# Kernel optimization log

Measured on AMD Instinct MI355X. Metric: run time of the kernel, lower is better.

The kernel has to match this reference:

```python
import jax, jax.numpy as jnp
import numpy as np

B, R, N, D_IN, D_OUT = 8, 4, 1024, 256, 256


def setup_inputs() -> dict:
    key = jax.random.key(0)
    k1, k2, k3, k4 = jax.random.split(key, 4)
    text = jax.random.normal(k1, (B, N, D_IN), dtype=jnp.float32)
    adj = jax.random.uniform(k2, (B, R, N, N), dtype=jnp.float32)
    weight = jax.random.normal(k3, (R, D_IN, D_OUT), dtype=jnp.float32) * 0.02
    bias = jax.random.normal(k4, (D_OUT,), dtype=jnp.float32) * 0.02
    return {"text": text, "adj": adj, "weight": weight, "bias": bias}


def reference(text, adj, weight, bias):
    # Row-normalize adjacency per relation (diag_embed+matmul in torch == row scale).
    rowsum = adj.sum(axis=-1)                                   # [B,R,N]
    r_inv = jnp.where(rowsum == 0, 0.0, 1.0 / rowsum)           # inf -> 0
    norm_adj = adj * r_inv[..., None]                           # [B,R,N,N]
    # Per-relation message passing, batched over relations.
    hidden = jnp.einsum('brij,bjd->brid', norm_adj, text)       # [B,R,N,D_in]
    # Concat over relations along feature dim: [B,N,R*D_in]
    tmp = jnp.transpose(hidden, (0, 2, 1, 3)).reshape(text.shape[0], text.shape[1], -1)
    w = weight.reshape(-1, weight.shape[-1])                    # [R*D_in, D_out]
    return tmp @ w + bias
```

## Files before the change

### kernel.cpp

```cpp
#include <hip/hip_runtime.h>
#include <hip/hip_bf16.h>
#include <stdint.h>

typedef __bf16 bf16_8 __attribute__((ext_vector_type(8)));
typedef float f32x4 __attribute__((ext_vector_type(4)));
typedef unsigned int u32;
typedef unsigned short u16;


__device__ __forceinline__ u16 f2b(float f) {
    return __builtin_bit_cast(u16, __float2bfloat16(f));
}

__device__ __forceinline__ u32 swz_off(u32 row, u32 g) {
    return (row * 4u + (g ^ ((row >> 1) & 3u))) * 16u;
}

__device__ __forceinline__ void gload_lds16(const void* g, void* l) {
    __builtin_amdgcn_global_load_lds((const __attribute__((address_space(1))) void*)g,
                                     (__attribute__((address_space(3))) void*)l, 16, 0, 0);
}

__device__ __forceinline__ void memfence_sched() { asm volatile("" ::: "memory"); }

__device__ __forceinline__ uint4 pack8(float4 a, float4 b) {
    uint4 pk;
    pk.x = (u32)f2b(a.x) | ((u32)f2b(a.y) << 16);
    pk.y = (u32)f2b(a.z) | ((u32)f2b(a.w) << 16);
    pk.z = (u32)f2b(b.x) | ((u32)f2b(b.y) << 16);
    pk.w = (u32)f2b(b.z) | ((u32)f2b(b.w) << 16);
    return pk;
}

template <int KSTEPS>
__device__ __forceinline__ void gemm_core(const u16* pA, u32 strideA,
                                          const u16* pB, u32 strideB,
                                          char* smem, f32x4 acc[4][4]) {
    const u32 t    = threadIdx.x;
    const u32 lane = t & 63u;
    const u32 w    = t >> 6;
    const u32 wm   = (w >> 1) * 64u;
    const u32 wn   = (w & 1u) * 64u;
    const u32 waveByte = (t & 192u) * 16u;
    const u32 row0 = t >> 2;
    const u32 gg0  = (t & 3u) ^ ((row0 >> 1) & 3u);
    const u32 row1 = row0 + 64u;
    const u32 gg1  = ((t + 256u) & 3u) ^ ((row1 >> 1) & 3u);
    const u32 fr = lane & 15u;
    const u32 fg = lane >> 4;

    gload_lds16(pA + (size_t)row0 * strideA + gg0 * 8u, smem + waveByte);
    gload_lds16(pA + (size_t)row1 * strideA + gg1 * 8u, smem + waveByte + 4096u);
    gload_lds16(pB + (size_t)row0 * strideB + gg0 * 8u, smem + 16384u + waveByte);
    gload_lds16(pB + (size_t)row1 * strideB + gg1 * 8u, smem + 16384u + waveByte + 4096u);
    asm volatile("s_waitcnt vmcnt(0)" ::: "memory");
    __builtin_amdgcn_s_barrier();

    u32 c = 0;
#pragma unroll 2
    for (int ks = 0; ks < KSTEPS; ++ks) {
        char* curA = smem + c * 8192u;
        char* curB = smem + 16384u + c * 8192u;
        if (ks + 1 < KSTEPS) {
            char* nxtA = smem + (c ^ 1u) * 8192u;
            char* nxtB = smem + 16384u + (c ^ 1u) * 8192u;
            const u32 k0 = (u32)(ks + 1) * 32u;
            gload_lds16(pA + (size_t)row0 * strideA + k0 + gg0 * 8u, nxtA + waveByte);
            gload_lds16(pA + (size_t)row1 * strideA + k0 + gg1 * 8u, nxtA + waveByte + 4096u);
            gload_lds16(pB + (size_t)row0 * strideB + k0 + gg0 * 8u, nxtB + waveByte);
            gload_lds16(pB + (size_t)row1 * strideB + k0 + gg1 * 8u, nxtB + waveByte + 4096u);
        }

        bf16_8 af[4], bfv[4];
#pragma unroll
        for (int mt = 0; mt < 4; ++mt) {
            uint4 v = *(const uint4*)(curA + swz_off(wm + (u32)mt * 16u + fr, fg));
            af[mt] = __builtin_bit_cast(bf16_8, v);
        }
#pragma unroll
        for (int nt = 0; nt < 4; ++nt) {
            uint4 v = *(const uint4*)(curB + swz_off(wn + (u32)nt * 16u + fr, fg));
            bfv[nt] = __builtin_bit_cast(bf16_8, v);
        }
#pragma unroll
        for (int mt = 0; mt < 4; ++mt)
#pragma unroll
            for (int nt = 0; nt < 4; ++nt)
                acc[mt][nt] = __builtin_amdgcn_mfma_f32_16x16x32_bf16(af[mt], bfv[nt],
                                                                      acc[mt][nt], 0, 0, 0);

        if (ks + 1 < KSTEPS) {
            asm volatile("s_waitcnt vmcnt(0)" ::: "memory");
            __builtin_amdgcn_s_barrier();
        }
        c ^= 1u;
    }
}

__global__ __launch_bounds__(256) void text_cvt_kernel(const float* t, u16* tb) {
    const u32 i8 = blockIdx.x * 256u + threadIdx.x;
    const float4 a = ((const float4*)t)[i8 * 2u];
    const float4 b = ((const float4*)t)[i8 * 2u + 1u];
    ((uint4*)tb)[i8] = pack8(a, b);
}

__global__ __launch_bounds__(256) void wt_cvt_kernel(const float* W, u16* Wt) {
    const u32 idx = blockIdx.x * 256u + threadIdx.x;
    const u32 r = idx >> 16, rem = idx & 65535u, dout = rem >> 8, din = rem & 255u;
    Wt[idx] = f2b(W[(r << 16) + (din << 8) + dout]);
}

__global__ __launch_bounds__(256) void y_gemm_kernel(const u16* Wt, const u16* textb,
                                                     u16* Yt) {
    __shared__ char smem[32768];
    const u32 bx = blockIdx.x;
    const u32 n0 = (bx & 7u) * 128u;
    const u32 m0 = ((bx >> 3) & 1u) * 128u;
    const u32 r  = (bx >> 4) & 3u;
    const u32 b  = bx >> 6;
    const u16* pA = Wt + (size_t)r * 65536u + (size_t)m0 * 256u;
    const u16* pB = textb + (size_t)b * 262144u + (size_t)n0 * 256u;
    f32x4 acc[4][4];
#pragma unroll
    for (int i = 0; i < 4; ++i)
#pragma unroll
        for (int j = 0; j < 4; ++j) acc[i][j] = (f32x4){0.f, 0.f, 0.f, 0.f};
    gemm_core<8>(pA, 256u, pB, 256u, smem, acc);

    const u32 lane = threadIdx.x & 63u, w = threadIdx.x >> 6;
    const u32 wm = (w >> 1) * 64u, wn = (w & 1u) * 64u;
    const u32 rit = (lane >> 4) * 4u, cit = lane & 15u;
    u16* yb = Yt + (size_t)(b * 4u + r) * 262144u;
#pragma unroll
    for (int mt = 0; mt < 4; ++mt)
#pragma unroll
        for (int nt = 0; nt < 4; ++nt) {
            const u32 m = m0 + wm + (u32)mt * 16u + rit;
            const u32 n = n0 + wn + (u32)nt * 16u + cit;
#pragma unroll
            for (int rg = 0; rg < 4; ++rg)
                yb[(size_t)(m + (u32)rg) * 1024u + n] = f2b(acc[mt][nt][rg]);
        }
}

__global__ __launch_bounds__(512, 4) void adj_gemm_partial(const float* adj,
                                                           const u16* Yt,
                                                           float* partial) {
    __shared__ char smem[57600];
    char* bufA = smem;
    char* bufB = smem + 8192;
    float* sInv = (float*)(smem + 57344);

    const u32 raw = blockIdx.x;
    const u32 bx = (raw & 7u) * 64u + (raw >> 3);

    const u32 i0 = (bx & 15u) * 64u;
    const u32 r  = (bx >> 4) & 3u;
    const u32 b  = bx >> 6;

    const float* pA = adj + (size_t)(b * 4u + r) * 1048576u + (size_t)i0 * 1024u;
    const u16*   pB = Yt + (size_t)(b * 4u + r) * 262144u;

    const u32 t    = threadIdx.x;
    const u32 lane = t & 63u;
    const u32 w    = t >> 6;
    const u32 wi   = (w >> 1) * 16u;
    const u32 wd   = (w & 1u) * 128u;
    const u32 fr   = lane & 15u;
    const u32 fg   = lane >> 4;

    const u32 arow = t >> 3;
    const u32 acg  = ((t >> 1) & 3u) ^ ((arow >> 1) & 3u);
    const float* aPtr = pA + (size_t)arow * 1024u + acg * 8u + (t & 1u) * 4u;

    const u32 brow0 = t >> 2;
    const u32 brow1 = (t + 512u) >> 2;
    const u32 bcg0  = (t & 3u) ^ ((brow0 >> 1) & 3u);
    const u32 bcg1  = (t & 3u) ^ ((brow1 >> 1) & 3u);
    const u16* bPtr0 = pB + (size_t)brow0 * 1024u + bcg0 * 8u;
    const u16* bPtr1 = pB + (size_t)brow1 * 1024u + bcg1 * 8u;
    const u32 waveB = (t & 448u) * 16u;

    f32x4 acc[8];
#pragma unroll
    for (int i = 0; i < 8; ++i) acc[i] = (f32x4){0.f, 0.f, 0.f, 0.f};

    float s0 = 0.f;
    float4 rA[2];

    auto stageB = [&](u32 kt, char* dst) {
        gload_lds16(bPtr0 + kt * 32u, dst + waveB);
        gload_lds16(bPtr1 + kt * 32u, dst + 8192u + waveB);
    };
    auto packA = [&](float4 a, char* dst) {
        s0 += (a.x + a.y) + (a.z + a.w);
        uint2 pk;
        pk.x = (u32)f2b(a.x) | ((u32)f2b(a.y) << 16);
        pk.y = (u32)f2b(a.z) | ((u32)f2b(a.w) << 16);
        *(uint2*)(dst + t * 8u) = pk;
    };
    auto do_mfma = [&](char* curA, char* curB) {
        uint4 va = *(const uint4*)(curA + swz_off(wi + fr, fg));
        bf16_8 af = __builtin_bit_cast(bf16_8, va);
#pragma unroll
        for (int nt = 0; nt < 8; ++nt) {
            uint4 v = *(const uint4*)(curB + swz_off(wd + (u32)nt * 16u + fr, fg));
            bf16_8 bfv = __builtin_bit_cast(bf16_8, v);
            acc[nt] = __builtin_amdgcn_mfma_f32_16x16x32_bf16(af, bfv, acc[nt], 0, 0, 0);
        }
    };

    rA[0] = *(const float4*)(aPtr);
    stageB(0u, bufB);
    memfence_sched();
    rA[1] = *(const float4*)(aPtr + 32u);
    stageB(1u, bufB + 16384u);
    memfence_sched();
    packA(rA[0], bufA);
    asm volatile("s_waitcnt vmcnt(3) lgkmcnt(0)" ::: "memory");
    __builtin_amdgcn_s_barrier();

#pragma unroll 6
    for (int ks = 0; ks < 30; ++ks) {
        const int cA = ks & 1;
        const int nA = cA ^ 1;

        packA(rA[nA], bufA + (u32)nA * 4096u);
        rA[cA] = *(const float4*)(aPtr + (u32)(ks + 2) * 32u);
        stageB((u32)(ks + 2), bufB + (u32)((ks + 2) % 3) * 16384u);

        do_mfma(bufA + (u32)cA * 4096u, bufB + (u32)(ks % 3) * 16384u);

        asm volatile("s_waitcnt vmcnt(3) lgkmcnt(0)" ::: "memory");
        __builtin_amdgcn_s_barrier();
    }

    packA(rA[1], bufA + 4096u);
    do_mfma(bufA, bufB);
    asm volatile("s_waitcnt vmcnt(0) lgkmcnt(0)" ::: "memory");
    __builtin_amdgcn_s_barrier();

    do_mfma(bufA + 4096u, bufB + 16384u);

    s0 += __shfl_down(s0, 4, 64);
    s0 += __shfl_down(s0, 2, 64);
    s0 += __shfl_down(s0, 1, 64);
    if ((t & 7u) == 0u) sInv[arow] = (s0 == 0.f) ? 0.f : 1.f / s0;
    __syncthreads();

    const u32 rit = fg * 4u;
    float* pp = partial + (size_t)(b * 4u + r) * 262144u + (size_t)i0 * 256u;
#pragma unroll
    for (int rg = 0; rg < 4; ++rg) {
        const u32 mRow = wi + rit + (u32)rg;
        const float inv = sInv[mRow];
#pragma unroll
        for (int nt = 0; nt < 8; ++nt)
            pp[(size_t)mRow * 256u + wd + (u32)nt * 16u + fr] = acc[nt][rg] * inv;
    }
}

__global__ __launch_bounds__(256) void reduce_kernel(const float* partial,
                                                     const float* bias, float* out) {
    const u32 i4 = blockIdx.x * 256u + threadIdx.x;
    const u32 base = i4 * 4u;
    const u32 b = base >> 18;
    const u32 rem = base & 262143u;
    float4 s = ((const float4*)bias)[i4 & 63u];
#pragma unroll
    for (u32 r = 0; r < 4; ++r) {
        const float4 v = *(const float4*)(partial + (((size_t)(b * 4u + r)) << 18) + rem);
        s.x += v.x; s.y += v.y; s.z += v.z; s.w += v.w;
    }
    ((float4*)out)[i4] = s;
}

extern "C" void kernel_launch(void* const* d_in, const int* in_sizes, int n_in,
                              void* d_out, int out_size, void* d_ws, size_t ws_size,
                              hipStream_t stream) {
    const float* text = (const float*)d_in[0];
    const float* adj  = (const float*)d_in[1];
    const float* wgt  = (const float*)d_in[2];
    const float* bias = (const float*)d_in[3];
    float* out = (float*)d_out;

    char* ws = (char*)d_ws;
    u16* Yt        = (u16*)ws;
    u16* textb     = (u16*)(ws + 16777216u);
    u16* Wt        = (u16*)(ws + 20971520u);
    float* partial = (float*)(ws + 21495808u);

    text_cvt_kernel<<<1024, 256, 0, stream>>>(text, textb);
    wt_cvt_kernel<<<1024, 256, 0, stream>>>(wgt, Wt);
    y_gemm_kernel<<<512, 256, 0, stream>>>(Wt, textb, Yt);
    adj_gemm_partial<<<512, 512, 0, stream>>>(adj, Yt, partial);
    reduce_kernel<<<2048, 256, 0, stream>>>(partial, bias, out);
}
```

Measured before the change: 67.09 us.

## Enlarge adj GEMM tile to 128x256 with K=64 phased pipeline

Rewrites the adjacency GEMM to use 128-row by 256-column tiles with a 64-wide K step, 8 waves in a 2x4 layout each computing 64x64. The main loop is split into four phases per K tile, with interleaved staging loads, barriers and s_setprio around the MFMA blocks. The goal is more reuse of the B operand per block and fewer K iterations. In exchange it uses 128KB of LDS and a lower occupancy target, and launches only 256 blocks, which may underfill the GPU's compute units.

```diff
diff --git a/kernel.cpp b/kernel.cpp
--- a/kernel.cpp
+++ b/kernel.cpp
@@ -14,6 +14,10 @@
 
 __device__ __forceinline__ u32 swz_off(u32 row, u32 g) {
     return (row * 4u + (g ^ ((row >> 1) & 3u))) * 16u;
+}
+
+__device__ __forceinline__ u32 swz8(u32 row, u32 c) {
+    return (row * 8u + (c ^ ((row >> 1) & 7u))) * 16u;
 }
 
 __device__ __forceinline__ void gload_lds16(const void* g, void* l) {
@@ -143,121 +147,166 @@
         }
 }
 
-__global__ __launch_bounds__(512, 4) void adj_gemm_partial(const float* adj,
-                                                           const u16* Yt,
-                                                           float* partial) {
-    __shared__ char smem[57600];
+__global__ __launch_bounds__(512, 2) void adj_gemm_8ph(const float* adj, const u16* Yt,
+                                                       float* partial) {
+    __shared__ char smem[131072];
     char* bufA = smem;
-    char* bufB = smem + 8192;
-    float* sInv = (float*)(smem + 57344);
+    char* bufB = smem + 32768;
+    float* sInv = (float*)smem;
 
     const u32 raw = blockIdx.x;
-    const u32 bx = (raw & 7u) * 64u + (raw >> 3);
-
-    const u32 i0 = (bx & 15u) * 64u;
-    const u32 r  = (bx >> 4) & 3u;
-    const u32 b  = bx >> 6;
+    const u32 bx = (raw & 7u) * 32u + (raw >> 3);
+    const u32 it = bx & 7u;
+    const u32 r  = (bx >> 3) & 3u;
+    const u32 b  = bx >> 5;
+    const u32 i0 = it * 128u;
 
     const float* pA = adj + (size_t)(b * 4u + r) * 1048576u + (size_t)i0 * 1024u;
     const u16*   pB = Yt + (size_t)(b * 4u + r) * 262144u;
 
-    const u32 t    = threadIdx.x;
-    const u32 lane = t & 63u;
-    const u32 w    = t >> 6;
-    const u32 wi   = (w >> 1) * 16u;
-    const u32 wd   = (w & 1u) * 128u;
-    const u32 fr   = lane & 15u;
-    const u32 fg   = lane >> 4;
-
-    const u32 arow = t >> 3;
-    const u32 acg  = ((t >> 1) & 3u) ^ ((arow >> 1) & 3u);
-    const float* aPtr = pA + (size_t)arow * 1024u + acg * 8u + (t & 1u) * 4u;
-
-    const u32 brow0 = t >> 2;
-    const u32 brow1 = (t + 512u) >> 2;
-    const u32 bcg0  = (t & 3u) ^ ((brow0 >> 1) & 3u);
-    const u32 bcg1  = (t & 3u) ^ ((brow1 >> 1) & 3u);
-    const u16* bPtr0 = pB + (size_t)brow0 * 1024u + bcg0 * 8u;
-    const u16* bPtr1 = pB + (size_t)brow1 * 1024u + bcg1 * 8u;
+    const u32 t = threadIdx.x, lane = t & 63u, w = t >> 6;
+    const u32 wm = (w >> 2) * 64u;
+    const u32 wn = (w & 3u) * 64u;
+    const u32 fr = lane & 15u, fg = lane >> 4;
+
+    const u32 sRow = t >> 2;
+    const float* aBase = pA + (size_t)sRow * 1024u + (t & 3u) * 16u;
+    const u32 aSw = (sRow >> 1) & 7u;
+    const u32 aSlot0 = (sRow * 8u + (((t & 3u) * 2u) ^ aSw)) * 16u;
+    const u32 aSlot1 = (sRow * 8u + (((t & 3u) * 2u + 1u) ^ aSw)) * 16u;
+
+    u32 bOff[4];
+#pragma unroll
+    for (int j = 0; j < 4; ++j) {
+        const u32 ci = (u32)j * 512u + t;
+        const u32 row = ci >> 3, g = ci & 7u;
+        bOff[j] = row * 1024u + (g ^ ((row >> 1) & 7u)) * 8u;
+    }
     const u32 waveB = (t & 448u) * 16u;
 
-    f32x4 acc[8];
-#pragma unroll
-    for (int i = 0; i < 8; ++i) acc[i] = (f32x4){0.f, 0.f, 0.f, 0.f};
+    f32x4 acc[4][4];
+#pragma unroll
+    for (int i = 0; i < 4; ++i)
+#pragma unroll
+        for (int j = 0; j < 4; ++j) acc[i][j] = (f32x4){0.f, 0.f, 0.f, 0.f};
 
     float s0 = 0.f;
-    float4 rA[2];
-
-    auto stageB = [&](u32 kt, char* dst) {
-        gload_lds16(bPtr0 + kt * 32u, dst + waveB);
-        gload_lds16(bPtr1 + kt * 32u, dst + 8192u + waveB);
+    float4 rA[2][4];
+
+    auto loadA = [&](float4* dst, u32 kt) {
+        const float* p = aBase + kt * 64u;
+        dst[0] = *(const float4*)(p);
+        dst[1] = *(const float4*)(p + 4);
+        dst[2] = *(const float4*)(p + 8);
+        dst[3] = *(const float4*)(p + 12);
     };
-    auto packA = [&](float4 a, char* dst) {
-        s0 += (a.x + a.y) + (a.z + a.w);
-        uint2 pk;
-        pk.x = (u32)f2b(a.x) | ((u32)f2b(a.y) << 16);
-        pk.y = (u32)f2b(a.z) | ((u32)f2b(a.w) << 16);
-        *(uint2*)(dst + t * 8u) = pk;
+    auto packA = [&](const float4* rs, char* dst) {
+        s0 += (rs[0].x + rs[0].y + rs[0].z + rs[0].w)
+            + (rs[1].x + rs[1].y + rs[1].z + rs[1].w)
+            + (rs[2].x + rs[2].y + rs[2].z + rs[2].w)
+            + (rs[3].x + rs[3].y + rs[3].z + rs[3].w);
+        *(uint4*)(dst + aSlot0) = pack8(rs[0], rs[1]);
+        *(uint4*)(dst + aSlot1) = pack8(rs[2], rs[3]);
     };
-    auto do_mfma = [&](char* curA, char* curB) {
-        uint4 va = *(const uint4*)(curA + swz_off(wi + fr, fg));
-        bf16_8 af = __builtin_bit_cast(bf16_8, va);
-#pragma unroll
-        for (int nt = 0; nt < 8; ++nt) {
-            uint4 v = *(const uint4*)(curB + swz_off(wd + (u32)nt * 16u + fr, fg));
-            bf16_8 bfv = __builtin_bit_cast(bf16_8, v);
-            acc[nt] = __builtin_amdgcn_mfma_f32_16x16x32_bf16(af, bfv, acc[nt], 0, 0, 0);
+
+    auto ktile = [&](char* bufAc, char* bufBc, char* bufAn, char* bufBn,
+                     float4* rIssue, const float4* rPack, u32 ktIss,
+                     bool doIssue, bool doPack, bool lastTile) {
+        bf16_8 af[4][2];
+#pragma unroll
+        for (int p = 0; p < 4; ++p) {
+            if (p == 0) {
+                if (doIssue) { loadA(rIssue, ktIss); memfence_sched(); }
+#pragma unroll
+                for (int mt = 0; mt < 4; ++mt)
+#pragma unroll
+                    for (int ks = 0; ks < 2; ++ks) {
+                        uint4 v = *(const uint4*)(bufAc +
+                                   swz8(wm + (u32)mt * 16u + fr, (u32)ks * 4u + fg));
+                        af[mt][ks] = __builtin_bit_cast(bf16_8, v);
+                    }
+            }
+            if (doIssue) {
+                gload_lds16(pB + bOff[p] + ktIss * 64u,
+                            bufBn + (u32)p * 8192u + waveB);
+                memfence_sched();
+            }
+            if (p == 3 && doPack) packA(rPack, bufAn);
+
+            bf16_8 bf[2];
+#pragma unroll
+            for (int ks = 0; ks < 2; ++ks) {
+                uint4 v = *(const uint4*)(bufBc +
+                           swz8(wn + (u32)p * 16u + fr, (u32)ks * 4u + fg));
+                bf[ks] = __builtin_bit_cast(bf16_8, v);
+            }
+            __builtin_amdgcn_s_barrier();
+            __builtin_amdgcn_s_setprio(1);
+#pragma unroll
+            for (int mt = 0; mt < 4; ++mt)
+#pragma unroll
+                for (int ks = 0; ks < 2; ++ks)
+                    acc[mt][p] = __builtin_amdgcn_mfma_f32_16x16x32_bf16(
+                        af[mt][ks], bf[ks], acc[mt][p], 0, 0, 0);
+            __builtin_amdgcn_s_setprio(0);
+            if (p < 3) {
+                __builtin_amdgcn_s_barrier();
+            } else {
+                if (doIssue)
+                    asm volatile("s_waitcnt vmcnt(8) lgkmcnt(0)" ::: "memory");
+                else if (doPack)
+                    asm volatile("s_waitcnt vmcnt(0) lgkmcnt(0)" ::: "memory");
+                else
+                    asm volatile("s_waitcnt lgkmcnt(0)" ::: "memory");
+                if (!lastTile) __builtin_amdgcn_s_barrier();
+            }
         }
     };
 
-    rA[0] = *(const float4*)(aPtr);
-    stageB(0u, bufB);
+    loadA(rA[0], 0u);
     memfence_sched();
-    rA[1] = *(const float4*)(aPtr + 32u);
-    stageB(1u, bufB + 16384u);
+#pragma unroll
+    for (int j = 0; j < 4; ++j)
+        gload_lds16(pB + bOff[j], bufB + (u32)j * 8192u + waveB);
+    memfence_sched();
+    loadA(rA[1], 1u);
+    memfence_sched();
+#pragma unroll
+    for (int j = 0; j < 4; ++j)
+        gload_lds16(pB + bOff[j] + 64u, bufB + 32768u + (u32)j * 8192u + waveB);
     memfence_sched();
     packA(rA[0], bufA);
-    asm volatile("s_waitcnt vmcnt(3) lgkmcnt(0)" ::: "memory");
+    asm volatile("s_waitcnt vmcnt(8) lgkmcnt(0)" ::: "memory");
     __builtin_amdgcn_s_barrier();
 
-#pragma unroll 6
-    for (int ks = 0; ks < 30; ++ks) {
-        const int cA = ks & 1;
-        const int nA = cA ^ 1;
-
-        packA(rA[nA], bufA + (u32)nA * 4096u);
-        rA[cA] = *(const float4*)(aPtr + (u32)(ks + 2) * 32u);
-        stageB((u32)(ks + 2), bufB + (u32)((ks + 2) % 3) * 16384u);
-
-        do_mfma(bufA + (u32)cA * 4096u, bufB + (u32)(ks % 3) * 16384u);
-
-        asm volatile("s_waitcnt vmcnt(3) lgkmcnt(0)" ::: "memory");
-        __builtin_amdgcn_s_barrier();
+#pragma unroll 2
+    for (int kt = 0; kt < 14; ++kt) {
+        const u32 cA = (u32)kt & 1u, nA = cA ^ 1u;
+        ktile(bufA + cA * 16384u, bufB + (u32)(kt % 3) * 32768u,
+              bufA + nA * 16384u, bufB + (u32)((kt + 2) % 3) * 32768u,
+              rA[cA], rA[nA], (u32)(kt + 2), true, true, false);
     }
-
-    packA(rA[1], bufA + 4096u);
-    do_mfma(bufA, bufB);
-    asm volatile("s_waitcnt vmcnt(0) lgkmcnt(0)" ::: "memory");
-    __builtin_amdgcn_s_barrier();
-
-    do_mfma(bufA + 4096u, bufB + 16384u);
-
-    s0 += __shfl_down(s0, 4, 64);
+    ktile(bufA, bufB + 2u * 32768u, bufA + 16384u, bufB,
+          rA[0], rA[1], 0u, false, true, false);
+    ktile(bufA + 16384u, bufB, bufA, bufB,
+          rA[0], rA[1], 0u, false, false, true);
+
     s0 += __shfl_down(s0, 2, 64);
     s0 += __shfl_down(s0, 1, 64);
-    if ((t & 7u) == 0u) sInv[arow] = (s0 == 0.f) ? 0.f : 1.f / s0;
+    if ((t & 3u) == 0u) sInv[sRow] = (s0 == 0.f) ? 0.f : 1.f / s0;
     __syncthreads();
 
-    const u32 rit = fg * 4u;
     float* pp = partial + (size_t)(b * 4u + r) * 262144u + (size_t)i0 * 256u;
 #pragma unroll
-    for (int rg = 0; rg < 4; ++rg) {
-        const u32 mRow = wi + rit + (u32)rg;
-        const float inv = sInv[mRow];
-#pragma unroll
-        for (int nt = 0; nt < 8; ++nt)
-            pp[(size_t)mRow * 256u + wd + (u32)nt * 16u + fr] = acc[nt][rg] * inv;
-    }
+    for (int mt = 0; mt < 4; ++mt)
+#pragma unroll
+        for (int rg = 0; rg < 4; ++rg) {
+            const u32 mRow = wm + (u32)mt * 16u + fg * 4u + (u32)rg;
+            const float inv = sInv[mRow];
+#pragma unroll
+            for (int nt = 0; nt < 4; ++nt)
+                pp[(size_t)mRow * 256u + wn + (u32)nt * 16u + fr] = acc[mt][nt][rg] * inv;
+        }
 }
 
 __global__ __launch_bounds__(256) void reduce_kernel(const float* partial,
@@ -293,6 +342,6 @@
     text_cvt_kernel<<<1024, 256, 0, stream>>>(text, textb);
     wt_cvt_kernel<<<1024, 256, 0, stream>>>(wgt, Wt);
     y_gemm_kernel<<<512, 256, 0, stream>>>(Wt, textb, Yt);
-    adj_gemm_partial<<<512, 512, 0, stream>>>(adj, Yt, partial);
+    adj_gemm_8ph<<<256, 512, 0, stream>>>(adj, Yt, partial);
     reduce_kernel<<<2048, 256, 0, stream>>>(partial, bias, out);
 }
```

New measurement: 82.04 us. 1.22x slower.

## Fuse relation reduction and bias into adj GEMM, drop reduce kernel

Applied to the files above, without the earlier changes.

Each block now processes a 32-row tile across all four relations sequentially, scaling each relation's result by its row-normalization and accumulating in registers before adding bias and writing the final output. This removes the fp32 partial buffer round trip and the separate reduce launch. In exchange the grid halves to 256 blocks with smaller tiles per block, reducing parallelism and per-iteration MFMA work relative to loads.

```diff
diff --git a/kernel.cpp b/kernel.cpp
--- a/kernel.cpp
+++ b/kernel.cpp
@@ -143,136 +143,120 @@
         }
 }
 
-__global__ __launch_bounds__(512, 4) void adj_gemm_partial(const float* adj,
-                                                           const u16* Yt,
-                                                           float* partial) {
-    __shared__ char smem[57600];
+__global__ __launch_bounds__(512, 2) void adj_gemm_out(const float* adj, const u16* Yt,
+                                                       const float* bias, float* out) {
+    __shared__ char smem[53376];
     char* bufA = smem;
-    char* bufB = smem + 8192;
-    float* sInv = (float*)(smem + 57344);
+    char* bufB = smem + 4096;
+    float* sInv = (float*)(smem + 53248);
 
     const u32 raw = blockIdx.x;
-    const u32 bx = (raw & 7u) * 64u + (raw >> 3);
-
-    const u32 i0 = (bx & 15u) * 64u;
-    const u32 r  = (bx >> 4) & 3u;
-    const u32 b  = bx >> 6;
-
-    const float* pA = adj + (size_t)(b * 4u + r) * 1048576u + (size_t)i0 * 1024u;
-    const u16*   pB = Yt + (size_t)(b * 4u + r) * 262144u;
-
-    const u32 t    = threadIdx.x;
-    const u32 lane = t & 63u;
-    const u32 w    = t >> 6;
-    const u32 wi   = (w >> 1) * 16u;
-    const u32 wd   = (w & 1u) * 128u;
-    const u32 fr   = lane & 15u;
-    const u32 fg   = lane >> 4;
-
-    const u32 arow = t >> 3;
-    const u32 acg  = ((t >> 1) & 3u) ^ ((arow >> 1) & 3u);
-    const float* aPtr = pA + (size_t)arow * 1024u + acg * 8u + (t & 1u) * 4u;
+    const u32 bx = (raw & 7u) * 32u + (raw >> 3);
+    const u32 i0 = (bx & 31u) * 32u;
+    const u32 b  = bx >> 5;
+
+    const u32 t = threadIdx.x, lane = t & 63u, w = t >> 6;
+    const u32 wi = (w >> 2) * 16u;
+    const u32 wd = (w & 3u) * 64u;
+    const u32 fr = lane & 15u, fg = lane >> 4;
+
+    const u32 sRow = t >> 4;
+    const u32 aKoff = (((t >> 2) & 3u) ^ ((sRow >> 1) & 3u)) * 8u + (t & 3u) * 2u;
 
     const u32 brow0 = t >> 2;
     const u32 brow1 = (t + 512u) >> 2;
-    const u32 bcg0  = (t & 3u) ^ ((brow0 >> 1) & 3u);
-    const u32 bcg1  = (t & 3u) ^ ((brow1 >> 1) & 3u);
-    const u16* bPtr0 = pB + (size_t)brow0 * 1024u + bcg0 * 8u;
-    const u16* bPtr1 = pB + (size_t)brow1 * 1024u + bcg1 * 8u;
+    const u32 bg0 = (t & 3u) ^ ((brow0 >> 1) & 3u);
+    const u32 bg1 = (t & 3u) ^ ((brow1 >> 1) & 3u);
     const u32 waveB = (t & 448u) * 16u;
 
-    f32x4 acc[8];
-#pragma unroll
-    for (int i = 0; i < 8; ++i) acc[i] = (f32x4){0.f, 0.f, 0.f, 0.f};
-
-    float s0 = 0.f;
-    float4 rA[2];
-
-    auto stageB = [&](u32 kt, char* dst) {
-        gload_lds16(bPtr0 + kt * 32u, dst + waveB);
-        gload_lds16(bPtr1 + kt * 32u, dst + 8192u + waveB);
-    };
-    auto packA = [&](float4 a, char* dst) {
-        s0 += (a.x + a.y) + (a.z + a.w);
-        uint2 pk;
-        pk.x = (u32)f2b(a.x) | ((u32)f2b(a.y) << 16);
-        pk.y = (u32)f2b(a.z) | ((u32)f2b(a.w) << 16);
-        *(uint2*)(dst + t * 8u) = pk;
-    };
-    auto do_mfma = [&](char* curA, char* curB) {
-        uint4 va = *(const uint4*)(curA + swz_off(wi + fr, fg));
-        bf16_8 af = __builtin_bit_cast(bf16_8, va);
-#pragma unroll
-        for (int nt = 0; nt < 8; ++nt) {
-            uint4 v = *(const uint4*)(curB + swz_off(wd + (u32)nt * 16u + fr, fg));
-            bf16_8 bfv = __builtin_bit_cast(bf16_8, v);
-            acc[nt] = __builtin_amdgcn_mfma_f32_16x16x32_bf16(af, bfv, acc[nt], 0, 0, 0);
-        }
-    };
-
-    rA[0] = *(const float4*)(aPtr);
-    stageB(0u, bufB);
-    memfence_sched();
-    rA[1] = *(const float4*)(aPtr + 32u);
-    stageB(1u, bufB + 16384u);
-    memfence_sched();
-    packA(rA[0], bufA);
-    asm volatile("s_waitcnt vmcnt(3) lgkmcnt(0)" ::: "memory");
-    __builtin_amdgcn_s_barrier();
-
-#pragma unroll 6
-    for (int ks = 0; ks < 30; ++ks) {
-        const int cA = ks & 1;
-        const int nA = cA ^ 1;
-
-        packA(rA[nA], bufA + (u32)nA * 4096u);
-        rA[cA] = *(const float4*)(aPtr + (u32)(ks + 2) * 32u);
-        stageB((u32)(ks + 2), bufB + (u32)((ks + 2) % 3) * 16384u);
-
-        do_mfma(bufA + (u32)cA * 4096u, bufB + (u32)(ks % 3) * 16384u);
-
+    f32x4 accT[4], accR[4];
+#pragma unroll
+    for (int i = 0; i < 4; ++i) accT[i] = (f32x4){0.f, 0.f, 0.f, 0.f};
+
+#pragma unroll 1
+    for (u32 r = 0; r < 4u; ++r) {
+        const float* pAr = adj + (((size_t)(b * 4u + r)) << 20) + (size_t)i0 * 1024u;
+        const u16*   pBr = Yt + (((size_t)(b * 4u + r)) << 18);
+        const float* aSrc = pAr + (size_t)sRow * 1024u + aKoff;
+        const u16* b0p = pBr + (size_t)brow0 * 1024u + bg0 * 8u;
+        const u16* b1p = pBr + (size_t)brow1 * 1024u + bg1 * 8u;
+
+#pragma unroll
+        for (int i = 0; i < 4; ++i) accR[i] = (f32x4){0.f, 0.f, 0.f, 0.f};
+        float s0 = 0.f;
+        float2 rA[2];
+
+        auto stageB = [&](u32 kt, char* dst) {
+            gload_lds16(b0p + kt * 32u, dst + waveB);
+            gload_lds16(b1p + kt * 32u, dst + 8192u + waveB);
+        };
+        auto packA = [&](float2 a, char* dst) {
+            s0 += a.x + a.y;
+            *(u32*)(dst + t * 4u) = (u32)f2b(a.x) | ((u32)f2b(a.y) << 16);
+        };
+        auto do_mfma = [&](char* curA, char* curB) {
+            uint4 va = *(const uint4*)(curA + swz_off(wi + fr, fg));
+            bf16_8 af = __builtin_bit_cast(bf16_8, va);
+#pragma unroll
+            for (int nt = 0; nt < 4; ++nt) {
+                uint4 v = *(const uint4*)(curB + swz_off(wd + (u32)nt * 16u + fr, fg));
+                bf16_8 bfv = __builtin_bit_cast(bf16_8, v);
+                accR[nt] = __builtin_amdgcn_mfma_f32_16x16x32_bf16(af, bfv, accR[nt],
+                                                                   0, 0, 0);
+            }
+        };
+
+        rA[0] = *(const float2*)(aSrc);
+        stageB(0u, bufB);
+        memfence_sched();
+        rA[1] = *(const float2*)(aSrc + 32u);
+        stageB(1u, bufB + 16384u);
+        memfence_sched();
+        packA(rA[0], bufA);
         asm volatile("s_waitcnt vmcnt(3) lgkmcnt(0)" ::: "memory");
         __builtin_amdgcn_s_barrier();
+
+#pragma unroll 6
+        for (int ks = 0; ks < 30; ++ks) {
+            const u32 cA = (u32)ks & 1u, nA = cA ^ 1u;
+            packA(rA[nA], bufA + nA * 2048u);
+            rA[cA] = *(const float2*)(aSrc + (u32)(ks + 2) * 32u);
+            stageB((u32)(ks + 2), bufB + (u32)((ks + 2) % 3) * 16384u);
+            do_mfma(bufA + cA * 2048u, bufB + (u32)(ks % 3) * 16384u);
+            asm volatile("s_waitcnt vmcnt(3) lgkmcnt(0)" ::: "memory");
+            __builtin_amdgcn_s_barrier();
+        }
+        packA(rA[1], bufA + 2048u);
+        do_mfma(bufA, bufB);
+        asm volatile("s_waitcnt vmcnt(0) lgkmcnt(0)" ::: "memory");
+        __builtin_amdgcn_s_barrier();
+        do_mfma(bufA + 2048u, bufB + 16384u);
+
+        s0 += __shfl_down(s0, 8, 16);
+        s0 += __shfl_down(s0, 4, 16);
+        s0 += __shfl_down(s0, 2, 16);
+        s0 += __shfl_down(s0, 1, 16);
+        if ((t & 15u) == 0u) sInv[sRow] = (s0 == 0.f) ? 0.f : 1.f / s0;
+        __syncthreads();
+#pragma unroll
+        for (int rg = 0; rg < 4; ++rg) {
+            const float inv = sInv[wi + fg * 4u + (u32)rg];
+#pragma unroll
+            for (int nt = 0; nt < 4; ++nt) accT[nt][rg] += accR[nt][rg] * inv;
+        }
     }
 
-    packA(rA[1], bufA + 4096u);
-    do_mfma(bufA, bufB);
-    asm volatile("s_waitcnt vmcnt(0) lgkmcnt(0)" ::: "memory");
-    __builtin_amdgcn_s_barrier();
-
-    do_mfma(bufA + 4096u, bufB + 16384u);
-
-    s0 += __shfl_down(s0, 4, 64);
-    s0 += __shfl_down(s0, 2, 64);
-    s0 += __shfl_down(s0, 1, 64);
-    if ((t & 7u) == 0u) sInv[arow] = (s0 == 0.f) ? 0.f : 1.f / s0;
-    __syncthreads();
-
-    const u32 rit = fg * 4u;
-    float* pp = partial + (size_t)(b * 4u + r) * 262144u + (size_t)i0 * 256u;
-#pragma unroll
-    for (int rg = 0; rg < 4; ++rg) {
-        const u32 mRow = wi + rit + (u32)rg;
-        const float inv = sInv[mRow];
-#pragma unroll
-        for (int nt = 0; nt < 8; ++nt)
-            pp[(size_t)mRow * 256u + wd + (u32)nt * 16u + fr] = acc[nt][rg] * inv;
+    float* ob = out + ((size_t)b << 18) + (size_t)i0 * 256u;
+#pragma unroll
+    for (int nt = 0; nt < 4; ++nt) {
+        const u32 col = wd + (u32)nt * 16u + fr;
+        const float bv = bias[col];
+#pragma unroll
+        for (int rg = 0; rg < 4; ++rg) {
+            const u32 mRow = wi + fg * 4u + (u32)rg;
+            ob[(size_t)mRow * 256u + col] = accT[nt][rg] + bv;
+        }
     }
-}
-
-__global__ __launch_bounds__(256) void reduce_kernel(const float* partial,
-                                                     const float* bias, float* out) {
-    const u32 i4 = blockIdx.x * 256u + threadIdx.x;
-    const u32 base = i4 * 4u;
-    const u32 b = base >> 18;
-    const u32 rem = base & 262143u;
-    float4 s = ((const float4*)bias)[i4 & 63u];
-#pragma unroll
-    for (u32 r = 0; r < 4; ++r) {
-        const float4 v = *(const float4*)(partial + (((size_t)(b * 4u + r)) << 18) + rem);
-        s.x += v.x; s.y += v.y; s.z += v.z; s.w += v.w;
-    }
-    ((float4*)out)[i4] = s;
 }
 
 extern "C" void kernel_launch(void* const* d_in, const int* in_sizes, int n_in,
@@ -285,14 +269,12 @@
     float* out = (float*)d_out;
 
     char* ws = (char*)d_ws;
-    u16* Yt        = (u16*)ws;
-    u16* textb     = (u16*)(ws + 16777216u);
-    u16* Wt        = (u16*)(ws + 20971520u);
-    float* partial = (float*)(ws + 21495808u);
+    u16* Yt    = (u16*)ws;
+    u16* textb = (u16*)(ws + 16777216u);
+    u16* Wt    = (u16*)(ws + 20971520u);
 
     text_cvt_kernel<<<1024, 256, 0, stream>>>(text, textb);
     wt_cvt_kernel<<<1024, 256, 0, stream>>>(wgt, Wt);
     y_gemm_kernel<<<512, 256, 0, stream>>>(Wt, textb, Yt);
-    adj_gemm_partial<<<512, 512, 0, stream>>>(adj, Yt, partial);
-    reduce_kernel<<<2048, 256, 0, stream>>>(partial, bias, out);
-}
+    adj_gemm_out<<<256, 512, 0, stream>>>(adj, Yt, bias, out);
+}
```

Result: slower. 108.8 us (+62.1%).

## Enlarge adj GEMM block tile to 128 rows with 4x4 per-wave MFMA tiles

Applied to the files above, without the earlier changes.

Each adj_gemm_partial block now covers 128 adjacency rows instead of 64, using a 2x4 wave layout where every wave computes a 64x64 tile with a 4x4 grid of MFMAs. The goal is to cut redundant reloads of the Yt operand, which halve because there are half as many blocks, and to raise the MFMA-to-LDS-read ratio per wave. The cost is larger LDS use, more accumulator registers, lower occupancy (launch bounds 2), and only 256 blocks, which may underfill the CUs. The pack8 helper is assumed to exist in the hidden part of the file.

```diff
diff --git a/kernel.cpp b/kernel.cpp
--- a/kernel.cpp
+++ b/kernel.cpp
@@ -143,121 +143,124 @@
         }
 }
 
-__global__ __launch_bounds__(512, 4) void adj_gemm_partial(const float* adj,
+__global__ __launch_bounds__(512, 2) void adj_gemm_partial(const float* adj,
                                                            const u16* Yt,
                                                            float* partial) {
-    __shared__ char smem[57600];
+    __shared__ char smem[66048];
     char* bufA = smem;
-    char* bufB = smem + 8192;
-    float* sInv = (float*)(smem + 57344);
+    char* bufB = smem + 16384;
+    float* sInv = (float*)(smem + 65536);
 
     const u32 raw = blockIdx.x;
-    const u32 bx = (raw & 7u) * 64u + (raw >> 3);
-
-    const u32 i0 = (bx & 15u) * 64u;
-    const u32 r  = (bx >> 4) & 3u;
-    const u32 b  = bx >> 6;
-
-    const float* pA = adj + (size_t)(b * 4u + r) * 1048576u + (size_t)i0 * 1024u;
-    const u16*   pB = Yt + (size_t)(b * 4u + r) * 262144u;
-
-    const u32 t    = threadIdx.x;
-    const u32 lane = t & 63u;
-    const u32 w    = t >> 6;
-    const u32 wi   = (w >> 1) * 16u;
-    const u32 wd   = (w & 1u) * 128u;
-    const u32 fr   = lane & 15u;
-    const u32 fg   = lane >> 4;
-
-    const u32 arow = t >> 3;
-    const u32 acg  = ((t >> 1) & 3u) ^ ((arow >> 1) & 3u);
-    const float* aPtr = pA + (size_t)arow * 1024u + acg * 8u + (t & 1u) * 4u;
+    const u32 bx = (raw & 7u) * 32u + (raw >> 3);
+    const u32 i0 = (bx & 7u) * 128u;
+    const u32 r  = (bx >> 3) & 3u;
+    const u32 b  = bx >> 5;
+
+    const float* pA = adj + (((size_t)(b * 4u + r)) << 20) + (size_t)i0 * 1024u;
+    const u16*   pB = Yt + (((size_t)(b * 4u + r)) << 18);
+
+    const u32 t = threadIdx.x, lane = t & 63u, w = t >> 6;
+    const u32 wm = (w >> 2) * 64u;
+    const u32 wn = (w & 3u) * 64u;
+    const u32 fr = lane & 15u, fg = lane >> 4;
+
+    const u32 sRow = t >> 2;
+    const u32 cSwz = (t & 3u) ^ ((sRow >> 1) & 3u);
+    const float* aSrc = pA + (size_t)sRow * 1024u + cSwz * 8u;
 
     const u32 brow0 = t >> 2;
     const u32 brow1 = (t + 512u) >> 2;
-    const u32 bcg0  = (t & 3u) ^ ((brow0 >> 1) & 3u);
-    const u32 bcg1  = (t & 3u) ^ ((brow1 >> 1) & 3u);
-    const u16* bPtr0 = pB + (size_t)brow0 * 1024u + bcg0 * 8u;
-    const u16* bPtr1 = pB + (size_t)brow1 * 1024u + bcg1 * 8u;
+    const u32 bg0 = (t & 3u) ^ ((brow0 >> 1) & 3u);
+    const u32 bg1 = (t & 3u) ^ ((brow1 >> 1) & 3u);
+    const u16* b0p = pB + (size_t)brow0 * 1024u + bg0 * 8u;
+    const u16* b1p = pB + (size_t)brow1 * 1024u + bg1 * 8u;
     const u32 waveB = (t & 448u) * 16u;
 
-    f32x4 acc[8];
-#pragma unroll
-    for (int i = 0; i < 8; ++i) acc[i] = (f32x4){0.f, 0.f, 0.f, 0.f};
+    f32x4 acc[4][4];
+#pragma unroll
+    for (int i = 0; i < 4; ++i)
+#pragma unroll
+        for (int j = 0; j < 4; ++j) acc[i][j] = (f32x4){0.f, 0.f, 0.f, 0.f};
 
     float s0 = 0.f;
-    float4 rA[2];
-
+    float4 rA[2][2];
+
+    auto loadA = [&](float4* dst, u32 kt) {
+        dst[0] = *(const float4*)(aSrc + kt * 32u);
+        dst[1] = *(const float4*)(aSrc + kt * 32u + 4u);
+    };
     auto stageB = [&](u32 kt, char* dst) {
-        gload_lds16(bPtr0 + kt * 32u, dst + waveB);
-        gload_lds16(bPtr1 + kt * 32u, dst + 8192u + waveB);
+        gload_lds16(b0p + kt * 32u, dst + waveB);
+        gload_lds16(b1p + kt * 32u, dst + 8192u + waveB);
     };
-    auto packA = [&](float4 a, char* dst) {
-        s0 += (a.x + a.y) + (a.z + a.w);
-        uint2 pk;
-        pk.x = (u32)f2b(a.x) | ((u32)f2b(a.y) << 16);
-        pk.y = (u32)f2b(a.z) | ((u32)f2b(a.w) << 16);
-        *(uint2*)(dst + t * 8u) = pk;
+    auto packA = [&](const float4* a2, char* dst) {
+        s0 += (a2[0].x + a2[0].y + a2[0].z + a2[0].w)
+            + (a2[1].x + a2[1].y + a2[1].z + a2[1].w);
+        *(uint4*)(dst + t * 16u) = pack8(a2[0], a2[1]);
     };
     auto do_mfma = [&](char* curA, char* curB) {
-        uint4 va = *(const uint4*)(curA + swz_off(wi + fr, fg));
-        bf16_8 af = __builtin_bit_cast(bf16_8, va);
-#pragma unroll
-        for (int nt = 0; nt < 8; ++nt) {
-            uint4 v = *(const uint4*)(curB + swz_off(wd + (u32)nt * 16u + fr, fg));
-            bf16_8 bfv = __builtin_bit_cast(bf16_8, v);
-            acc[nt] = __builtin_amdgcn_mfma_f32_16x16x32_bf16(af, bfv, acc[nt], 0, 0, 0);
-        }
+        bf16_8 af[4], bfv[4];
+#pragma unroll
+        for (int mt = 0; mt < 4; ++mt) {
+            uint4 v = *(const uint4*)(curA + swz_off(wm + (u32)mt * 16u + fr, fg));
+            af[mt] = __builtin_bit_cast(bf16_8, v);
+        }
+#pragma unroll
+        for (int nt = 0; nt < 4; ++nt) {
+            uint4 v = *(const uint4*)(curB + swz_off(wn + (u32)nt * 16u + fr, fg));
+            bfv[nt] = __builtin_bit_cast(bf16_8, v);
+        }
+#pragma unroll
+        for (int mt = 0; mt < 4; ++mt)
+#pragma unroll
+            for (int nt = 0; nt < 4; ++nt)
+                acc[mt][nt] = __builtin_amdgcn_mfma_f32_16x16x32_bf16(af[mt], bfv[nt],
+                                                                      acc[mt][nt], 0, 0, 0);
     };
 
-    rA[0] = *(const float4*)(aPtr);
+    loadA(rA[0], 0u);
     stageB(0u, bufB);
     memfence_sched();
-    rA[1] = *(const float4*)(aPtr + 32u);
+    loadA(rA[1], 1u);
     stageB(1u, bufB + 16384u);
     memfence_sched();
     packA(rA[0], bufA);
-    asm volatile("s_waitcnt vmcnt(3) lgkmcnt(0)" ::: "memory");
+    asm volatile("s_waitcnt vmcnt(4) lgkmcnt(0)" ::: "memory");
     __builtin_amdgcn_s_barrier();
 
 #pragma unroll 6
     for (int ks = 0; ks < 30; ++ks) {
-        const int cA = ks & 1;
-        const int nA = cA ^ 1;
-
-        packA(rA[nA], bufA + (u32)nA * 4096u);
-        rA[cA] = *(const float4*)(aPtr + (u32)(ks + 2) * 32u);
+        const u32 cA = (u32)ks & 1u, nA = cA ^ 1u;
+        packA(rA[nA], bufA + nA * 8192u);
+        loadA(rA[cA], (u32)(ks + 2));
         stageB((u32)(ks + 2), bufB + (u32)((ks + 2) % 3) * 16384u);
-
-        do_mfma(bufA + (u32)cA * 4096u, bufB + (u32)(ks % 3) * 16384u);
-
-        asm volatile("s_waitcnt vmcnt(3) lgkmcnt(0)" ::: "memory");
+        do_mfma(bufA + cA * 8192u, bufB + (u32)(ks % 3) * 16384u);
+        asm volatile("s_waitcnt vmcnt(4) lgkmcnt(0)" ::: "memory");
         __builtin_amdgcn_s_barrier();
     }
-
-    packA(rA[1], bufA + 4096u);
+    packA(rA[1], bufA + 8192u);
     do_mfma(bufA, bufB);
     asm volatile("s_waitcnt vmcnt(0) lgkmcnt(0)" ::: "memory");
     __builtin_amdgcn_s_barrier();
-
-    do_mfma(bufA + 4096u, bufB + 16384u);
-
-    s0 += __shfl_down(s0, 4, 64);
+    do_mfma(bufA + 8192u, bufB + 16384u);
+
     s0 += __shfl_down(s0, 2, 64);
     s0 += __shfl_down(s0, 1, 64);
-    if ((t & 7u) == 0u) sInv[arow] = (s0 == 0.f) ? 0.f : 1.f / s0;
+    if ((t & 3u) == 0u) sInv[sRow] = (s0 == 0.f) ? 0.f : 1.f / s0;
     __syncthreads();
 
-    const u32 rit = fg * 4u;
-    float* pp = partial + (size_t)(b * 4u + r) * 262144u + (size_t)i0 * 256u;
-#pragma unroll
-    for (int rg = 0; rg < 4; ++rg) {
-        const u32 mRow = wi + rit + (u32)rg;
-        const float inv = sInv[mRow];
-#pragma unroll
-        for (int nt = 0; nt < 8; ++nt)
-            pp[(size_t)mRow * 256u + wd + (u32)nt * 16u + fr] = acc[nt][rg] * inv;
-    }
+    float* pp = partial + (((size_t)(b * 4u + r)) << 18) + (size_t)i0 * 256u;
+#pragma unroll
+    for (int mt = 0; mt < 4; ++mt)
+#pragma unroll
+        for (int rg = 0; rg < 4; ++rg) {
+            const u32 mRow = wm + (u32)mt * 16u + fg * 4u + (u32)rg;
+            const float inv = sInv[mRow];
+#pragma unroll
+            for (int nt = 0; nt < 4; ++nt)
+                pp[(size_t)mRow * 256u + wn + (u32)nt * 16u + fr] = acc[mt][nt][rg] * inv;
+        }
 }
 
 __global__ __launch_bounds__(256) void reduce_kernel(const float* partial,
@@ -293,6 +296,6 @@
     text_cvt_kernel<<<1024, 256, 0, stream>>>(text, textb);
     wt_cvt_kernel<<<1024, 256, 0, stream>>>(wgt, Wt);
     y_gemm_kernel<<<512, 256, 0, stream>>>(Wt, textb, Yt);
-    adj_gemm_partial<<<512, 512, 0, stream>>>(adj, Yt, partial);
+    adj_gemm_partial<<<256, 512, 0, stream>>>(adj, Yt, partial);
     reduce_kernel<<<2048, 256, 0, stream>>>(partial, bias, out);
 }
```

After: 66.06 us. About the same (-1.5%).
